# Kernel optimization log

Measured on AMD Instinct MI355X. Metric: run time of the kernel, lower is better.

The kernel has to match this reference:

```python
import jax, jax.numpy as jnp
import numpy as np


def setup_inputs() -> dict:
    key = jax.random.key(0)
    ks = jax.random.split(key, 8)
    n_videos, emb_dim = 200000, 128
    n_nodes, k_neigh = 20000, 32
    sc = 1.0 / np.sqrt(emb_dim)
    return {
        "video_embeddings": jax.random.normal(ks[0], (n_videos, emb_dim), jnp.float32),
        "video_nodes": jax.random.randint(ks[1], (n_nodes,), 0, n_videos, jnp.int64 if jax.config.jax_enable_x64 else jnp.int32),
        "neigh_idx": jax.random.randint(ks[2], (n_nodes, k_neigh), 0, n_videos, jnp.int64 if jax.config.jax_enable_x64 else jnp.int32),
        "W1": jax.random.normal(ks[3], (2 * emb_dim, emb_dim), jnp.float32) * sc,
        "b1": jnp.zeros((emb_dim,), jnp.float32),
        "W2": jax.random.normal(ks[4], (emb_dim, emb_dim), jnp.float32) * sc,
        "b2": jnp.zeros((emb_dim,), jnp.float32),
        "W3": jax.random.normal(ks[5], (emb_dim, 1), jnp.float32) * sc,
        "b3": jnp.zeros((1,), jnp.float32),
    }


def reference(video_embeddings, video_nodes, neigh_idx, W1, b1, W2, b2, W3, b3):
    # Ragged per-node loop vectorized as a padded [N, K] neighbor gather.
    neigh_emb = video_embeddings[neigh_idx]          # [N, K, D]
    node_emb = video_embeddings[video_nodes]         # [N, D]
    n, k, d = neigh_emb.shape
    # Attention MLP: cat(neigh, node_repeated) -> relu -> relu -> scalar score
    x = jnp.concatenate([neigh_emb, jnp.broadcast_to(node_emb[:, None, :], (n, k, d))], axis=-1)  # [N, K, 2D]
    h = jax.nn.relu(jnp.einsum("nke,ed->nkd", x, W1) + b1)
    h = jax.nn.relu(jnp.einsum("nke,ed->nkd", h, W2) + b2)
    scores = (jnp.einsum("nkd,do->nko", h, W3) + b3)[..., 0]  # [N, K]
    att = jax.nn.softmax(scores, axis=-1)                      # softmax over neighbors
    # Weighted aggregation: embed_matrix[i] = neigh_emb[i].T @ att[i]
    return jnp.einsum("nkd,nk->nd", neigh_emb, att)
```

## Files before the change

kernel.cpp:

```cpp
#include <hip/hip_runtime.h>
#include <hip/hip_bf16.h>

#define D  128
#define KN 32

typedef __attribute__((ext_vector_type(8))) short bf16x8;
typedef __attribute__((ext_vector_type(4))) float f32x4;

static __device__ __forceinline__ unsigned short f2bf(float f) {
    union { float f; unsigned int u; } v; v.f = f;
    unsigned int u = v.u;
    u += 0x7fff + ((u >> 16) & 1);
    return (unsigned short)(u >> 16);
}
static __device__ __forceinline__ float bf2f(unsigned short h) {
    union { float f; unsigned int u; } v; v.u = ((unsigned int)h) << 16;
    return v.f;
}

__global__ __launch_bounds__(256) void wt_kernel(
    const float* __restrict__ W1, const float* __restrict__ W2,
    unsigned short* __restrict__ W1Tt, unsigned short* __restrict__ W1Tb,
    unsigned short* __restrict__ W2T)
{
    int idx = blockIdx.x * 256 + threadIdx.x;
    if (idx < D * D) {
        int col = idx >> 7, e = idx & 127;
        W1Tt[col * D + e] = f2bf(W1[e * D + col]);
        W1Tb[col * D + e] = f2bf(W1[(D + e) * D + col]);
        W2T [col * D + e] = f2bf(W2[e * D + col]);
    }
}

__global__ __launch_bounds__(256) void p1q_kernel(
    const float* __restrict__ emb, const int* __restrict__ gidx, int M,
    const unsigned short* __restrict__ WT, const float* __restrict__ bias,
    unsigned short* __restrict__ dst)
{
    __shared__ unsigned short sA[128][136];

    const int tid  = threadIdx.x;
    const int lane = tid & 63;
    const int w    = tid >> 6;
    const int m    = lane & 15, q = lane >> 4;
    const int r0   = blockIdx.x * 128;

#pragma unroll
    for (int i = 0; i < 16; ++i) {
        int e = tid + 256 * i;
        int row = e >> 5, c4 = (e & 31) << 2;
        int r = r0 + row; if (r > M - 1) r = M - 1;
        int vr = gidx ? gidx[r] : r;
        const float4 f = *(const float4*)(emb + (long)vr * D + c4);
        ushort4 h;
        h.x = f2bf(f.x); h.y = f2bf(f.y); h.z = f2bf(f.z); h.w = f2bf(f.w);
        *(ushort4*)(&sA[row][c4]) = h;
    }
    __syncthreads();

    bf16x8 Bf[2][4];
#pragma unroll
    for (int nt = 0; nt < 2; ++nt)
#pragma unroll
        for (int kk = 0; kk < 4; ++kk)
            Bf[nt][kk] = *(const bf16x8*)(WT + (32 * w + 16 * nt + m) * D + kk * 32 + q * 8);
    float bv[2];
#pragma unroll
    for (int nt = 0; nt < 2; ++nt) bv[nt] = bias ? bias[32 * w + 16 * nt + m] : 0.f;

    f32x4 acc[8][2];
#pragma unroll
    for (int mt = 0; mt < 8; ++mt)
#pragma unroll
        for (int nt = 0; nt < 2; ++nt) acc[mt][nt] = (f32x4){0.f, 0.f, 0.f, 0.f};

#pragma unroll
    for (int kk = 0; kk < 4; ++kk) {
        bf16x8 a[8];
#pragma unroll
        for (int mt = 0; mt < 8; ++mt)
            a[mt] = *(const bf16x8*)(&sA[16 * mt + m][kk * 32 + q * 8]);
#pragma unroll
        for (int mt = 0; mt < 8; ++mt) {
            acc[mt][0] = __builtin_amdgcn_mfma_f32_16x16x32_bf16(a[mt], Bf[0][kk], acc[mt][0], 0, 0, 0);
            acc[mt][1] = __builtin_amdgcn_mfma_f32_16x16x32_bf16(a[mt], Bf[1][kk], acc[mt][1], 0, 0, 0);
        }
    }

#pragma unroll
    for (int mt = 0; mt < 8; ++mt)
#pragma unroll
        for (int nt = 0; nt < 2; ++nt) {
            int col = 32 * w + 16 * nt + m;
#pragma unroll
            for (int r = 0; r < 4; ++r) {
                int row = r0 + 16 * mt + 4 * q + r;
                if (row < M) dst[(long)row * D + col] = f2bf(acc[mt][nt][r] + bv[nt]);
            }
        }
}

__global__ __launch_bounds__(256) void agg_kernel(
    const float* __restrict__ emb,
    const int* __restrict__ nidx,
    const unsigned short* __restrict__ W2T,
    const float* __restrict__ b2, const float* __restrict__ W3,
    const float* __restrict__ b3,
    const unsigned short* __restrict__ P1, const unsigned short* __restrict__ Q,
    float* __restrict__ out, int NN)
{
    __shared__ unsigned short sX[64][136];
    __shared__ int   sIdx[64];
    __shared__ float sSp[4][64];
    __shared__ float sAtt[64];

    const int tid  = threadIdx.x;
    const int lane = tid & 63;
    const int w    = tid >> 6;
    const int m    = lane & 15, q = lane >> 4;

    bf16x8 Bf[2][4];
#pragma unroll
    for (int nt = 0; nt < 2; ++nt)
#pragma unroll
        for (int kk = 0; kk < 4; ++kk)
            Bf[nt][kk] = *(const bf16x8*)(W2T + (32 * w + 16 * nt + m) * D + kk * 32 + q * 8);
    float b2v[2], w3v[2];
#pragma unroll
    for (int nt = 0; nt < 2; ++nt) {
        int col = 32 * w + 16 * nt + m;
        b2v[nt] = b2[col];
        w3v[nt] = W3[col];
    }
    const float b3s = b3[0];

    const int pairs = (NN + 1) >> 1;
    for (int pr = blockIdx.x; pr < pairs; pr += gridDim.x) {
        const int node0 = pr * 2;

        {
            int row = tid >> 2, t4 = tid & 3;
            int nd = node0 + (row >> 5); if (nd > NN - 1) nd = NN - 1;
            int k = row & 31;
            int ni = nidx[nd * KN + k];
            if (t4 == 0) sIdx[row] = ni;
            const bf16x8* pp = (const bf16x8*)(P1 + (long)ni * D);
            const bf16x8* qq = (const bf16x8*)(Q + (long)nd * D);
#pragma unroll
            for (int j = 0; j < 4; ++j) {
                int c = t4 * 4 + j;
                bf16x8 p = pp[c], qv = qq[c], r;
#pragma unroll
                for (int h = 0; h < 8; ++h) {
                    float v = bf2f((unsigned short)p[h]) + bf2f((unsigned short)qv[h]);
                    r[h] = (short)f2bf(v > 0.f ? v : 0.f);
                }
                *(bf16x8*)(&sX[row][c * 8]) = r;
            }
        }
        __syncthreads();

        f32x4 acc[4][2];
#pragma unroll
        for (int mt = 0; mt < 4; ++mt)
#pragma unroll
            for (int nt = 0; nt < 2; ++nt) acc[mt][nt] = (f32x4){0.f, 0.f, 0.f, 0.f};

#pragma unroll
        for (int kk = 0; kk < 4; ++kk) {
            bf16x8 a[4];
#pragma unroll
            for (int mt = 0; mt < 4; ++mt)
                a[mt] = *(const bf16x8*)(&sX[16 * mt + m][kk * 32 + q * 8]);
#pragma unroll
            for (int mt = 0; mt < 4; ++mt) {
                acc[mt][0] = __builtin_amdgcn_mfma_f32_16x16x32_bf16(a[mt], Bf[0][kk], acc[mt][0], 0, 0, 0);
                acc[mt][1] = __builtin_amdgcn_mfma_f32_16x16x32_bf16(a[mt], Bf[1][kk], acc[mt][1], 0, 0, 0);
            }
        }

#pragma unroll
        for (int mt = 0; mt < 4; ++mt) {
            float p[4];
#pragma unroll
            for (int r = 0; r < 4; ++r) {
                float h0 = acc[mt][0][r] + b2v[0]; h0 = h0 > 0.f ? h0 : 0.f;
                float h1 = acc[mt][1][r] + b2v[1]; h1 = h1 > 0.f ? h1 : 0.f;
                p[r] = h0 * w3v[0] + h1 * w3v[1];
            }
#pragma unroll
            for (int off = 8; off >= 1; off >>= 1)
#pragma unroll
                for (int r = 0; r < 4; ++r) p[r] += __shfl_xor(p[r], off, 16);
            if (m == 0) {
#pragma unroll
                for (int r = 0; r < 4; ++r) sSp[w][16 * mt + 4 * q + r] = p[r];
            }
        }
        __syncthreads();

        if (tid < 64) {
            float s = sSp[0][tid] + sSp[1][tid] + sSp[2][tid] + sSp[3][tid] + b3s;
            float mx = s;
#pragma unroll
            for (int off = 16; off >= 1; off >>= 1) mx = fmaxf(mx, __shfl_xor(mx, off, 32));
            float e = __expf(s - mx);
            float sum = e;
#pragma unroll
            for (int off = 16; off >= 1; off >>= 1) sum += __shfl_xor(sum, off, 32);
            sAtt[tid] = e / sum;
        }
        __syncthreads();

        {
            int ln = tid >> 7, dcol = tid & 127;
            float a = 0.f;
#pragma unroll
            for (int k = 0; k < KN; ++k)
                a += sAtt[ln * KN + k] * emb[(long)sIdx[ln * KN + k] * D + dcol];
            int nd = node0 + ln;
            if (nd < NN) out[(long)nd * D + dcol] = a;
        }
        __syncthreads();
    }
}

__global__ __launch_bounds__(128) void naive_kernel(
    const float* __restrict__ emb, const int* __restrict__ vnodes,
    const int* __restrict__ nidx,
    const float* __restrict__ W1, const float* __restrict__ b1,
    const float* __restrict__ W2, const float* __restrict__ b2,
    const float* __restrict__ W3, const float* __restrict__ b3,
    float* __restrict__ out)
{
    __shared__ float sE[KN + 1][D];
    __shared__ float sH[KN][D];
    __shared__ float sH2[KN][D];
    __shared__ float sS[KN];
    __shared__ float sA2[KN];
    const int node = blockIdx.x, tid = threadIdx.x;

    for (int r = 0; r < KN + 1; ++r) {
        int vr = (r < KN) ? nidx[node * KN + r] : vnodes[node];
        sE[r][tid] = emb[(long)vr * D + tid];
    }
    __syncthreads();
    for (int k = 0; k < KN; ++k) {
        float s = b1[tid];
        for (int e = 0; e < D; ++e) s += sE[k][e]  * W1[e * D + tid];
        for (int e = 0; e < D; ++e) s += sE[KN][e] * W1[(D + e) * D + tid];
        sH[k][tid] = s > 0.f ? s : 0.f;
    }
    __syncthreads();
    for (int k = 0; k < KN; ++k) {
        float s = b2[tid];
        for (int e = 0; e < D; ++e) s += sH[k][e] * W2[e * D + tid];
        sH2[k][tid] = s > 0.f ? s : 0.f;
    }
    __syncthreads();
    if (tid < KN) {
        float s = b3[0];
        for (int e = 0; e < D; ++e) s += sH2[tid][e] * W3[e];
        sS[tid] = s;
    }
    __syncthreads();
    if (tid == 0) {
        float mx = sS[0];
        for (int k = 1; k < KN; ++k) mx = fmaxf(mx, sS[k]);
        float sum = 0.f;
        for (int k = 0; k < KN; ++k) { sA2[k] = __expf(sS[k] - mx); sum += sA2[k]; }
        for (int k = 0; k < KN; ++k) sA2[k] /= sum;
    }
    __syncthreads();
    float a = 0.f;
    for (int k = 0; k < KN; ++k) a += sA2[k] * sE[k][tid];
    out[(long)node * D + tid] = a;
}

extern "C" void kernel_launch(void* const* d_in, const int* in_sizes, int n_in,
                              void* d_out, int out_size, void* d_ws, size_t ws_size,
                              hipStream_t stream) {
    const float* emb    = (const float*)d_in[0];
    const int*   vnodes = (const int*)d_in[1];
    const int*   nidx   = (const int*)d_in[2];
    const float* W1     = (const float*)d_in[3];
    const float* b1     = (const float*)d_in[4];
    const float* W2     = (const float*)d_in[5];
    const float* b2     = (const float*)d_in[6];
    const float* W3     = (const float*)d_in[7];
    const float* b3     = (const float*)d_in[8];
    float* out = (float*)d_out;

    const int NV = in_sizes[0] / D;
    const int NN = in_sizes[1];

    const size_t p1_elems = (size_t)NV * D;
    const size_t q_elems  = (size_t)NN * D;
    const size_t wt_elems = (size_t)D * D;
    const size_t need = (p1_elems + q_elems + 3 * wt_elems) * sizeof(unsigned short);

    if (ws_size >= need) {
        unsigned short* P1   = (unsigned short*)d_ws;
        unsigned short* Q    = P1 + p1_elems;
        unsigned short* W1Tt = Q + q_elems;
        unsigned short* W1Tb = W1Tt + wt_elems;
        unsigned short* W2T  = W1Tb + wt_elems;
        wt_kernel<<<(D * D + 255) / 256, 256, 0, stream>>>(W1, W2, W1Tt, W1Tb, W2T);
        p1q_kernel<<<(NV + 127) / 128, 256, 0, stream>>>(emb, nullptr, NV, W1Tt, nullptr, P1);
        p1q_kernel<<<(NN + 127) / 128, 256, 0, stream>>>(emb, vnodes, NN, W1Tb, b1, Q);
        agg_kernel<<<2048, 256, 0, stream>>>(emb, nidx, W2T, b2, W3, b3, P1, Q, out, NN);
    } else {
        naive_kernel<<<NN, D, 0, stream>>>(emb, vnodes, nidx, W1, b1, W2, b2, W3, b3, out);
    }
}
```

Baseline: 325.9 us.

## Gather bf16 embedding copy in aggregation and process four nodes per block

The P1 GEMM kernel now also writes a bf16 copy of the embedding table from its shared-memory tile. The aggregation kernel gathers neighbor rows from that copy, prefetching them into registers before the MFMA stage, which halves gather bytes. The kernel now handles four nodes per block iteration with larger shared buffers and an occupancy hint. The cost is an extra 200000x128 bf16 write, more workspace, and lower-precision weighted aggregation.

```diff
diff --git a/kernel.cpp b/kernel.cpp
--- a/kernel.cpp
+++ b/kernel.cpp
@@ -35,7 +35,7 @@
 __global__ __launch_bounds__(256) void p1q_kernel(
     const float* __restrict__ emb, const int* __restrict__ gidx, int M,
     const unsigned short* __restrict__ WT, const float* __restrict__ bias,
-    unsigned short* __restrict__ dst)
+    unsigned short* __restrict__ dst, unsigned short* __restrict__ EB)
 {
     __shared__ unsigned short sA[128][136];
 
@@ -58,6 +58,16 @@
     }
     __syncthreads();
 
+    if (EB) {
+        int row = tid >> 1, half = tid & 1;
+        if (r0 + row < M) {
+#pragma unroll
+            for (int j = 0; j < 8; ++j)
+                *(bf16x8*)(EB + (long)(r0 + row) * D + half * 64 + j * 8) =
+                    *(const bf16x8*)(&sA[row][half * 64 + j * 8]);
+        }
+    }
+
     bf16x8 Bf[2][4];
 #pragma unroll
     for (int nt = 0; nt < 2; ++nt)
@@ -76,14 +86,11 @@
 
 #pragma unroll
     for (int kk = 0; kk < 4; ++kk) {
-        bf16x8 a[8];
-#pragma unroll
-        for (int mt = 0; mt < 8; ++mt)
-            a[mt] = *(const bf16x8*)(&sA[16 * mt + m][kk * 32 + q * 8]);
 #pragma unroll
         for (int mt = 0; mt < 8; ++mt) {
-            acc[mt][0] = __builtin_amdgcn_mfma_f32_16x16x32_bf16(a[mt], Bf[0][kk], acc[mt][0], 0, 0, 0);
-            acc[mt][1] = __builtin_amdgcn_mfma_f32_16x16x32_bf16(a[mt], Bf[1][kk], acc[mt][1], 0, 0, 0);
+            bf16x8 a = *(const bf16x8*)(&sA[16 * mt + m][kk * 32 + q * 8]);
+            acc[mt][0] = __builtin_amdgcn_mfma_f32_16x16x32_bf16(a, Bf[0][kk], acc[mt][0], 0, 0, 0);
+            acc[mt][1] = __builtin_amdgcn_mfma_f32_16x16x32_bf16(a, Bf[1][kk], acc[mt][1], 0, 0, 0);
         }
     }
 
@@ -100,8 +107,9 @@
         }
 }
 
-__global__ __launch_bounds__(256) void agg_kernel(
-    const float* __restrict__ emb,
+template <bool USE_EB>
+__global__ __launch_bounds__(256, 3) void agg_kernel(
+    const float* __restrict__ emb, const unsigned short* __restrict__ EB,
     const int* __restrict__ nidx,
     const unsigned short* __restrict__ W2T,
     const float* __restrict__ b2, const float* __restrict__ W3,
@@ -109,10 +117,10 @@
     const unsigned short* __restrict__ P1, const unsigned short* __restrict__ Q,
     float* __restrict__ out, int NN)
 {
-    __shared__ unsigned short sX[64][136];
-    __shared__ int   sIdx[64];
-    __shared__ float sSp[4][64];
-    __shared__ float sAtt[64];
+    __shared__ unsigned short sX[128][136];
+    __shared__ int   sIdx[128];
+    __shared__ float sSp[4][128];
+    __shared__ float sAtt[128];
 
     const int tid  = threadIdx.x;
     const int lane = tid & 63;
@@ -134,53 +142,59 @@
     }
     const float b3s = b3[0];
 
-    const int pairs = (NN + 1) >> 1;
-    for (int pr = blockIdx.x; pr < pairs; pr += gridDim.x) {
-        const int node0 = pr * 2;
+    const int groups = (NN + 3) >> 2;
+    for (int g = blockIdx.x; g < groups; g += gridDim.x) {
+        const int node0 = g * 4;
 
         {
-            int row = tid >> 2, t4 = tid & 3;
+            int row = tid >> 1, half = tid & 1;
             int nd = node0 + (row >> 5); if (nd > NN - 1) nd = NN - 1;
             int k = row & 31;
             int ni = nidx[nd * KN + k];
-            if (t4 == 0) sIdx[row] = ni;
-            const bf16x8* pp = (const bf16x8*)(P1 + (long)ni * D);
-            const bf16x8* qq = (const bf16x8*)(Q + (long)nd * D);
-#pragma unroll
-            for (int j = 0; j < 4; ++j) {
-                int c = t4 * 4 + j;
-                bf16x8 p = pp[c], qv = qq[c], r;
+            if (half == 0) sIdx[row] = ni;
+            const bf16x8* pp = (const bf16x8*)(P1 + (long)ni * D) + half * 8;
+            const bf16x8* qq = (const bf16x8*)(Q + (long)nd * D) + half * 8;
+#pragma unroll
+            for (int j = 0; j < 8; ++j) {
+                bf16x8 p = pp[j], qv = qq[j], r;
 #pragma unroll
                 for (int h = 0; h < 8; ++h) {
                     float v = bf2f((unsigned short)p[h]) + bf2f((unsigned short)qv[h]);
                     r[h] = (short)f2bf(v > 0.f ? v : 0.f);
                 }
-                *(bf16x8*)(&sX[row][c * 8]) = r;
+                *(bf16x8*)(&sX[row][half * 64 + j * 8]) = r;
             }
         }
         __syncthreads();
 
-        f32x4 acc[4][2];
-#pragma unroll
-        for (int mt = 0; mt < 4; ++mt)
+        bf16x8 gv[8];
+        if (USE_EB) {
+#pragma unroll
+            for (int j = 0; j < 8; ++j) {
+                int k = (lane >> 4) + 4 * j;
+                int ni = sIdx[w * KN + k];
+                gv[j] = *(const bf16x8*)(EB + (long)ni * D + (lane & 15) * 8);
+            }
+        }
+
+        f32x4 acc[8][2];
+#pragma unroll
+        for (int mt = 0; mt < 8; ++mt)
 #pragma unroll
             for (int nt = 0; nt < 2; ++nt) acc[mt][nt] = (f32x4){0.f, 0.f, 0.f, 0.f};
 
 #pragma unroll
         for (int kk = 0; kk < 4; ++kk) {
-            bf16x8 a[4];
-#pragma unroll
-            for (int mt = 0; mt < 4; ++mt)
-                a[mt] = *(const bf16x8*)(&sX[16 * mt + m][kk * 32 + q * 8]);
-#pragma unroll
-            for (int mt = 0; mt < 4; ++mt) {
-                acc[mt][0] = __builtin_amdgcn_mfma_f32_16x16x32_bf16(a[mt], Bf[0][kk], acc[mt][0], 0, 0, 0);
-                acc[mt][1] = __builtin_amdgcn_mfma_f32_16x16x32_bf16(a[mt], Bf[1][kk], acc[mt][1], 0, 0, 0);
-            }
-        }
-
-#pragma unroll
-        for (int mt = 0; mt < 4; ++mt) {
+#pragma unroll
+            for (int mt = 0; mt < 8; ++mt) {
+                bf16x8 a = *(const bf16x8*)(&sX[16 * mt + m][kk * 32 + q * 8]);
+                acc[mt][0] = __builtin_amdgcn_mfma_f32_16x16x32_bf16(a, Bf[0][kk], acc[mt][0], 0, 0, 0);
+                acc[mt][1] = __builtin_amdgcn_mfma_f32_16x16x32_bf16(a, Bf[1][kk], acc[mt][1], 0, 0, 0);
+            }
+        }
+
+#pragma unroll
+        for (int mt = 0; mt < 8; ++mt) {
             float p[4];
 #pragma unroll
             for (int r = 0; r < 4; ++r) {
@@ -199,7 +213,7 @@
         }
         __syncthreads();
 
-        if (tid < 64) {
+        if (tid < 128) {
             float s = sSp[0][tid] + sSp[1][tid] + sSp[2][tid] + sSp[3][tid] + b3s;
             float mx = s;
 #pragma unroll
@@ -212,14 +226,40 @@
         }
         __syncthreads();
 
-        {
-            int ln = tid >> 7, dcol = tid & 127;
-            float a = 0.f;
-#pragma unroll
-            for (int k = 0; k < KN; ++k)
-                a += sAtt[ln * KN + k] * emb[(long)sIdx[ln * KN + k] * D + dcol];
-            int nd = node0 + ln;
-            if (nd < NN) out[(long)nd * D + dcol] = a;
+        if (USE_EB) {
+            float r[8] = {0.f, 0.f, 0.f, 0.f, 0.f, 0.f, 0.f, 0.f};
+#pragma unroll
+            for (int j = 0; j < 8; ++j) {
+                float a = sAtt[w * KN + (lane >> 4) + 4 * j];
+#pragma unroll
+                for (int h = 0; h < 8; ++h)
+                    r[h] += a * bf2f((unsigned short)gv[j][h]);
+            }
+#pragma unroll
+            for (int h = 0; h < 8; ++h) {
+                r[h] += __shfl_xor(r[h], 16);
+                r[h] += __shfl_xor(r[h], 32);
+            }
+            int nd = node0 + w;
+            if (lane < 16 && nd < NN) {
+                float4 o0 = {r[0], r[1], r[2], r[3]};
+                float4 o1 = {r[4], r[5], r[6], r[7]};
+                *(float4*)(out + (long)nd * D + lane * 8)     = o0;
+                *(float4*)(out + (long)nd * D + lane * 8 + 4) = o1;
+            }
+        } else {
+            float a0 = 0.f, a1 = 0.f;
+            for (int k = 0; k < KN; ++k) {
+                float att = sAtt[w * KN + k];
+                const float* er = emb + (long)sIdx[w * KN + k] * D;
+                a0 += att * er[lane];
+                a1 += att * er[lane + 64];
+            }
+            int nd = node0 + w;
+            if (nd < NN) {
+                out[(long)nd * D + lane]      = a0;
+                out[(long)nd * D + lane + 64] = a1;
+            }
         }
         __syncthreads();
     }
@@ -297,18 +337,25 @@
     const size_t p1_elems = (size_t)NV * D;
     const size_t q_elems  = (size_t)NN * D;
     const size_t wt_elems = (size_t)D * D;
-    const size_t need = (p1_elems + q_elems + 3 * wt_elems) * sizeof(unsigned short);
-
-    if (ws_size >= need) {
+    const size_t base_elems = p1_elems + q_elems + 3 * wt_elems;
+    const size_t need_base = base_elems * sizeof(unsigned short);
+    const size_t need_eb   = (base_elems + p1_elems) * sizeof(unsigned short);
+
+    if (ws_size >= need_base) {
         unsigned short* P1   = (unsigned short*)d_ws;
         unsigned short* Q    = P1 + p1_elems;
         unsigned short* W1Tt = Q + q_elems;
         unsigned short* W1Tb = W1Tt + wt_elems;
         unsigned short* W2T  = W1Tb + wt_elems;
+        unsigned short* EB   = (ws_size >= need_eb) ? (W2T + wt_elems) : nullptr;
+
         wt_kernel<<<(D * D + 255) / 256, 256, 0, stream>>>(W1, W2, W1Tt, W1Tb, W2T);
-        p1q_kernel<<<(NV + 127) / 128, 256, 0, stream>>>(emb, nullptr, NV, W1Tt, nullptr, P1);
-        p1q_kernel<<<(NN + 127) / 128, 256, 0, stream>>>(emb, vnodes, NN, W1Tb, b1, Q);
-        agg_kernel<<<2048, 256, 0, stream>>>(emb, nidx, W2T, b2, W3, b3, P1, Q, out, NN);
+        p1q_kernel<<<(NV + 127) / 128, 256, 0, stream>>>(emb, nullptr, NV, W1Tt, nullptr, P1, EB);
+        p1q_kernel<<<(NN + 127) / 128, 256, 0, stream>>>(emb, vnodes, NN, W1Tb, b1, Q, nullptr);
+        if (EB)
+            agg_kernel<true><<<2048, 256, 0, stream>>>(emb, EB, nidx, W2T, b2, W3, b3, P1, Q, out, NN);
+        else
+            agg_kernel<false><<<2048, 256, 0, stream>>>(emb, nullptr, nidx, W2T, b2, W3, b3, P1, Q, out, NN);
     } else {
         naive_kernel<<<NN, D, 0, stream>>>(emb, vnodes, nidx, W1, b1, W2, b2, W3, b3, out);
     }
```

New measurement: 315.4 us. -3.2%, faster.

## Merge projection launches, emit bf16 embeddings, and process one node per wave

Applied to the files above, without the earlier changes.

The two projection launches are merged into a single grid. The NV branch also writes a bf16 copy of the embedding table, and the A tiles are loaded straight from global memory instead of going through shared memory. The aggregation kernel now gives each wave its own node, so it needs no shared memory or block barriers. The softmax and weighted sum run entirely in registers with shuffles, and the weighted sum reads the half-size bf16 embeddings. This cuts fp32 gather traffic and synchronisation, at the cost of an extra bf16 table write, bf16 precision in the aggregation, and dropping b3 (harmless, since softmax is shift-invariant).

```diff
diff --git a/kernel.cpp b/kernel.cpp
--- a/kernel.cpp
+++ b/kernel.cpp
@@ -16,6 +16,12 @@
 static __device__ __forceinline__ float bf2f(unsigned short h) {
     union { float f; unsigned int u; } v; v.u = ((unsigned int)h) << 16;
     return v.f;
+}
+static __device__ __forceinline__ float bflo(unsigned int u) {
+    union { float f; unsigned int u; } v; v.u = u << 16; return v.f;
+}
+static __device__ __forceinline__ float bfhi(unsigned int u) {
+    union { float f; unsigned int u; } v; v.u = u & 0xffff0000u; return v.f;
 }
 
 __global__ __launch_bounds__(256) void wt_kernel(
@@ -33,196 +39,189 @@
 }
 
 __global__ __launch_bounds__(256) void p1q_kernel(
-    const float* __restrict__ emb, const int* __restrict__ gidx, int M,
-    const unsigned short* __restrict__ WT, const float* __restrict__ bias,
-    unsigned short* __restrict__ dst)
+    const float* __restrict__ emb, const int* __restrict__ vnodes,
+    int NV, int NN, int nvBlocks,
+    const unsigned short* __restrict__ W1Tt, const unsigned short* __restrict__ W1Tb,
+    const float* __restrict__ b1,
+    unsigned short* __restrict__ P1, unsigned short* __restrict__ Q,
+    unsigned short* __restrict__ EB)
 {
-    __shared__ unsigned short sA[128][136];
-
     const int tid  = threadIdx.x;
     const int lane = tid & 63;
     const int w    = tid >> 6;
     const int m    = lane & 15, q = lane >> 4;
-    const int r0   = blockIdx.x * 128;
-
-#pragma unroll
-    for (int i = 0; i < 16; ++i) {
-        int e = tid + 256 * i;
-        int row = e >> 5, c4 = (e & 31) << 2;
-        int r = r0 + row; if (r > M - 1) r = M - 1;
-        int vr = gidx ? gidx[r] : r;
-        const float4 f = *(const float4*)(emb + (long)vr * D + c4);
-        ushort4 h;
-        h.x = f2bf(f.x); h.y = f2bf(f.y); h.z = f2bf(f.z); h.w = f2bf(f.w);
-        *(ushort4*)(&sA[row][c4]) = h;
-    }
-    __syncthreads();
-
-    bf16x8 Bf[2][4];
-#pragma unroll
-    for (int nt = 0; nt < 2; ++nt)
-#pragma unroll
-        for (int kk = 0; kk < 4; ++kk)
-            Bf[nt][kk] = *(const bf16x8*)(WT + (32 * w + 16 * nt + m) * D + kk * 32 + q * 8);
-    float bv[2];
-#pragma unroll
-    for (int nt = 0; nt < 2; ++nt) bv[nt] = bias ? bias[32 * w + 16 * nt + m] : 0.f;
-
-    f32x4 acc[8][2];
-#pragma unroll
-    for (int mt = 0; mt < 8; ++mt)
-#pragma unroll
-        for (int nt = 0; nt < 2; ++nt) acc[mt][nt] = (f32x4){0.f, 0.f, 0.f, 0.f};
+
+    const bool nv = (int)blockIdx.x < nvBlocks;
+    const int  bi = nv ? blockIdx.x : blockIdx.x - nvBlocks;
+    const int  M  = nv ? NV : NN;
+    const unsigned short* WT = nv ? W1Tt : W1Tb;
+    unsigned short* dst = nv ? P1 : Q;
+    const int r0w = bi * 128 + w * 32;
+
+    int row[2], vr[2];
+#pragma unroll
+    for (int mt = 0; mt < 2; ++mt) {
+        int r = r0w + 16 * mt + m;
+        row[mt] = r < M ? r : M - 1;
+        vr[mt]  = nv ? row[mt] : vnodes[row[mt]];
+    }
+
+    f32x4 acc[2][8];
+#pragma unroll
+    for (int mt = 0; mt < 2; ++mt)
+#pragma unroll
+        for (int nt = 0; nt < 8; ++nt) acc[mt][nt] = (f32x4){0.f, 0.f, 0.f, 0.f};
 
 #pragma unroll
     for (int kk = 0; kk < 4; ++kk) {
-        bf16x8 a[8];
-#pragma unroll
-        for (int mt = 0; mt < 8; ++mt)
-            a[mt] = *(const bf16x8*)(&sA[16 * mt + m][kk * 32 + q * 8]);
-#pragma unroll
-        for (int mt = 0; mt < 8; ++mt) {
-            acc[mt][0] = __builtin_amdgcn_mfma_f32_16x16x32_bf16(a[mt], Bf[0][kk], acc[mt][0], 0, 0, 0);
-            acc[mt][1] = __builtin_amdgcn_mfma_f32_16x16x32_bf16(a[mt], Bf[1][kk], acc[mt][1], 0, 0, 0);
-        }
-    }
-
-#pragma unroll
-    for (int mt = 0; mt < 8; ++mt)
-#pragma unroll
-        for (int nt = 0; nt < 2; ++nt) {
-            int col = 32 * w + 16 * nt + m;
+        bf16x8 a[2];
+#pragma unroll
+        for (int mt = 0; mt < 2; ++mt) {
+            const float* src = emb + (long)vr[mt] * D + kk * 32 + q * 8;
+            float4 f0 = *(const float4*)src;
+            float4 f1 = *(const float4*)(src + 4);
+            a[mt][0] = (short)f2bf(f0.x); a[mt][1] = (short)f2bf(f0.y);
+            a[mt][2] = (short)f2bf(f0.z); a[mt][3] = (short)f2bf(f0.w);
+            a[mt][4] = (short)f2bf(f1.x); a[mt][5] = (short)f2bf(f1.y);
+            a[mt][6] = (short)f2bf(f1.z); a[mt][7] = (short)f2bf(f1.w);
+            if (nv && EB)
+                *(bf16x8*)(EB + (long)row[mt] * D + kk * 32 + q * 8) = a[mt];
+        }
+#pragma unroll
+        for (int nt = 0; nt < 8; ++nt) {
+            bf16x8 b = *(const bf16x8*)(WT + (16 * nt + m) * D + kk * 32 + q * 8);
+            acc[0][nt] = __builtin_amdgcn_mfma_f32_16x16x32_bf16(a[0], b, acc[0][nt], 0, 0, 0);
+            acc[1][nt] = __builtin_amdgcn_mfma_f32_16x16x32_bf16(a[1], b, acc[1][nt], 0, 0, 0);
+        }
+    }
+
+    float bv[8];
+#pragma unroll
+    for (int nt = 0; nt < 8; ++nt) bv[nt] = nv ? 0.f : b1[16 * nt + m];
+
+#pragma unroll
+    for (int mt = 0; mt < 2; ++mt)
+#pragma unroll
+        for (int nt = 0; nt < 8; ++nt)
 #pragma unroll
             for (int r = 0; r < 4; ++r) {
-                int row = r0 + 16 * mt + 4 * q + r;
-                if (row < M) dst[(long)row * D + col] = f2bf(acc[mt][nt][r] + bv[nt]);
+                int orow = r0w + 16 * mt + 4 * q + r;
+                if (orow < M)
+                    dst[(long)orow * D + 16 * nt + m] = f2bf(acc[mt][nt][r] + bv[nt]);
             }
-        }
 }
 
 __global__ __launch_bounds__(256) void agg_kernel(
-    const float* __restrict__ emb,
-    const int* __restrict__ nidx,
-    const unsigned short* __restrict__ W2T,
-    const float* __restrict__ b2, const float* __restrict__ W3,
-    const float* __restrict__ b3,
+    const unsigned short* __restrict__ EB, const int* __restrict__ nidx,
+    const unsigned short* __restrict__ W2T, const float* __restrict__ b2,
+    const float* __restrict__ W3,
     const unsigned short* __restrict__ P1, const unsigned short* __restrict__ Q,
     float* __restrict__ out, int NN)
 {
-    __shared__ unsigned short sX[64][136];
-    __shared__ int   sIdx[64];
-    __shared__ float sSp[4][64];
-    __shared__ float sAtt[64];
-
-    const int tid  = threadIdx.x;
-    const int lane = tid & 63;
-    const int w    = tid >> 6;
+    const int lane = threadIdx.x & 63;
+    const int w    = threadIdx.x >> 6;
     const int m    = lane & 15, q = lane >> 4;
-
-    bf16x8 Bf[2][4];
-#pragma unroll
-    for (int nt = 0; nt < 2; ++nt)
-#pragma unroll
-        for (int kk = 0; kk < 4; ++kk)
-            Bf[nt][kk] = *(const bf16x8*)(W2T + (32 * w + 16 * nt + m) * D + kk * 32 + q * 8);
-    float b2v[2], w3v[2];
-#pragma unroll
-    for (int nt = 0; nt < 2; ++nt) {
-        int col = 32 * w + 16 * nt + m;
-        b2v[nt] = b2[col];
-        w3v[nt] = W3[col];
-    }
-    const float b3s = b3[0];
-
-    const int pairs = (NN + 1) >> 1;
-    for (int pr = blockIdx.x; pr < pairs; pr += gridDim.x) {
-        const int node0 = pr * 2;
-
-        {
-            int row = tid >> 2, t4 = tid & 3;
-            int nd = node0 + (row >> 5); if (nd > NN - 1) nd = NN - 1;
-            int k = row & 31;
-            int ni = nidx[nd * KN + k];
-            if (t4 == 0) sIdx[row] = ni;
-            const bf16x8* pp = (const bf16x8*)(P1 + (long)ni * D);
-            const bf16x8* qq = (const bf16x8*)(Q + (long)nd * D);
-#pragma unroll
-            for (int j = 0; j < 4; ++j) {
-                int c = t4 * 4 + j;
-                bf16x8 p = pp[c], qv = qq[c], r;
-#pragma unroll
-                for (int h = 0; h < 8; ++h) {
-                    float v = bf2f((unsigned short)p[h]) + bf2f((unsigned short)qv[h]);
-                    r[h] = (short)f2bf(v > 0.f ? v : 0.f);
-                }
-                *(bf16x8*)(&sX[row][c * 8]) = r;
+    const int nd   = blockIdx.x * 4 + w;
+    if (nd >= NN) return;
+
+    const int idxv = nidx[nd * KN + (lane & 31)];
+    const int r0 = __shfl(idxv, m);
+    const int r1 = __shfl(idxv, 16 + m);
+
+    unsigned int ek[KN];
+#pragma unroll
+    for (int k = 0; k < KN; ++k) {
+        int ik = __shfl(idxv, k);
+        ek[k] = *(const unsigned int*)(EB + (long)ik * D + lane * 2);
+    }
+
+    float b2v[8], w3v[8];
+#pragma unroll
+    for (int nt = 0; nt < 8; ++nt) {
+        b2v[nt] = b2[16 * nt + m];
+        w3v[nt] = W3[16 * nt + m];
+    }
+
+    f32x4 acc[2][8];
+#pragma unroll
+    for (int mt = 0; mt < 2; ++mt)
+#pragma unroll
+        for (int nt = 0; nt < 8; ++nt) acc[mt][nt] = (f32x4){0.f, 0.f, 0.f, 0.f};
+
+#pragma unroll
+    for (int kk = 0; kk < 4; ++kk) {
+        bf16x8 qv = *(const bf16x8*)(Q  + (long)nd * D + kk * 32 + q * 8);
+        bf16x8 p0 = *(const bf16x8*)(P1 + (long)r0 * D + kk * 32 + q * 8);
+        bf16x8 p1 = *(const bf16x8*)(P1 + (long)r1 * D + kk * 32 + q * 8);
+        bf16x8 a0, a1;
+#pragma unroll
+        for (int h = 0; h < 8; ++h) {
+            float v0 = bf2f((unsigned short)p0[h]) + bf2f((unsigned short)qv[h]);
+            float v1 = bf2f((unsigned short)p1[h]) + bf2f((unsigned short)qv[h]);
+            a0[h] = (short)f2bf(v0 > 0.f ? v0 : 0.f);
+            a1[h] = (short)f2bf(v1 > 0.f ? v1 : 0.f);
+        }
+#pragma unroll
+        for (int nt = 0; nt < 8; ++nt) {
+            bf16x8 b = *(const bf16x8*)(W2T + (16 * nt + m) * D + kk * 32 + q * 8);
+            acc[0][nt] = __builtin_amdgcn_mfma_f32_16x16x32_bf16(a0, b, acc[0][nt], 0, 0, 0);
+            acc[1][nt] = __builtin_amdgcn_mfma_f32_16x16x32_bf16(a1, b, acc[1][nt], 0, 0, 0);
+        }
+    }
+
+    float att[2][4];
+#pragma unroll
+    for (int mt = 0; mt < 2; ++mt)
+#pragma unroll
+        for (int r = 0; r < 4; ++r) {
+            float p = 0.f;
+#pragma unroll
+            for (int nt = 0; nt < 8; ++nt) {
+                float h = acc[mt][nt][r] + b2v[nt];
+                p += (h > 0.f ? h : 0.f) * w3v[nt];
             }
-        }
-        __syncthreads();
-
-        f32x4 acc[4][2];
-#pragma unroll
-        for (int mt = 0; mt < 4; ++mt)
-#pragma unroll
-            for (int nt = 0; nt < 2; ++nt) acc[mt][nt] = (f32x4){0.f, 0.f, 0.f, 0.f};
-
-#pragma unroll
-        for (int kk = 0; kk < 4; ++kk) {
-            bf16x8 a[4];
-#pragma unroll
-            for (int mt = 0; mt < 4; ++mt)
-                a[mt] = *(const bf16x8*)(&sX[16 * mt + m][kk * 32 + q * 8]);
-#pragma unroll
-            for (int mt = 0; mt < 4; ++mt) {
-                acc[mt][0] = __builtin_amdgcn_mfma_f32_16x16x32_bf16(a[mt], Bf[0][kk], acc[mt][0], 0, 0, 0);
-                acc[mt][1] = __builtin_amdgcn_mfma_f32_16x16x32_bf16(a[mt], Bf[1][kk], acc[mt][1], 0, 0, 0);
-            }
-        }
-
-#pragma unroll
-        for (int mt = 0; mt < 4; ++mt) {
-            float p[4];
-#pragma unroll
-            for (int r = 0; r < 4; ++r) {
-                float h0 = acc[mt][0][r] + b2v[0]; h0 = h0 > 0.f ? h0 : 0.f;
-                float h1 = acc[mt][1][r] + b2v[1]; h1 = h1 > 0.f ? h1 : 0.f;
-                p[r] = h0 * w3v[0] + h1 * w3v[1];
-            }
-#pragma unroll
-            for (int off = 8; off >= 1; off >>= 1)
-#pragma unroll
-                for (int r = 0; r < 4; ++r) p[r] += __shfl_xor(p[r], off, 16);
-            if (m == 0) {
-#pragma unroll
-                for (int r = 0; r < 4; ++r) sSp[w][16 * mt + 4 * q + r] = p[r];
-            }
-        }
-        __syncthreads();
-
-        if (tid < 64) {
-            float s = sSp[0][tid] + sSp[1][tid] + sSp[2][tid] + sSp[3][tid] + b3s;
-            float mx = s;
-#pragma unroll
-            for (int off = 16; off >= 1; off >>= 1) mx = fmaxf(mx, __shfl_xor(mx, off, 32));
-            float e = __expf(s - mx);
-            float sum = e;
-#pragma unroll
-            for (int off = 16; off >= 1; off >>= 1) sum += __shfl_xor(sum, off, 32);
-            sAtt[tid] = e / sum;
-        }
-        __syncthreads();
-
-        {
-            int ln = tid >> 7, dcol = tid & 127;
-            float a = 0.f;
-#pragma unroll
-            for (int k = 0; k < KN; ++k)
-                a += sAtt[ln * KN + k] * emb[(long)sIdx[ln * KN + k] * D + dcol];
-            int nd = node0 + ln;
-            if (nd < NN) out[(long)nd * D + dcol] = a;
-        }
-        __syncthreads();
-    }
+            att[mt][r] = p;
+        }
+#pragma unroll
+    for (int off = 1; off <= 8; off <<= 1)
+#pragma unroll
+        for (int mt = 0; mt < 2; ++mt)
+#pragma unroll
+            for (int r = 0; r < 4; ++r)
+                att[mt][r] += __shfl_xor(att[mt][r], off);
+
+    float mx = att[0][0];
+#pragma unroll
+    for (int mt = 0; mt < 2; ++mt)
+#pragma unroll
+        for (int r = 0; r < 4; ++r) mx = fmaxf(mx, att[mt][r]);
+    mx = fmaxf(mx, __shfl_xor(mx, 16));
+    mx = fmaxf(mx, __shfl_xor(mx, 32));
+    float sum = 0.f;
+#pragma unroll
+    for (int mt = 0; mt < 2; ++mt)
+#pragma unroll
+        for (int r = 0; r < 4; ++r) {
+            att[mt][r] = __expf(att[mt][r] - mx);
+            sum += att[mt][r];
+        }
+    sum += __shfl_xor(sum, 16);
+    sum += __shfl_xor(sum, 32);
+    const float inv = 1.f / sum;
+#pragma unroll
+    for (int mt = 0; mt < 2; ++mt)
+#pragma unroll
+        for (int r = 0; r < 4; ++r) att[mt][r] *= inv;
+
+    float ox = 0.f, oy = 0.f;
+#pragma unroll
+    for (int k = 0; k < KN; ++k) {
+        float a = __shfl(att[k >> 4][k & 3], ((k >> 2) & 3) << 4);
+        ox += a * bflo(ek[k]);
+        oy += a * bfhi(ek[k]);
+    }
+    float2 o = {ox, oy};
+    *(float2*)(out + (long)nd * D + lane * 2) = o;
 }
 
 __global__ __launch_bounds__(128) void naive_kernel(
@@ -297,7 +296,7 @@
     const size_t p1_elems = (size_t)NV * D;
     const size_t q_elems  = (size_t)NN * D;
     const size_t wt_elems = (size_t)D * D;
-    const size_t need = (p1_elems + q_elems + 3 * wt_elems) * sizeof(unsigned short);
+    const size_t need = (2 * p1_elems + q_elems + 3 * wt_elems) * sizeof(unsigned short);
 
     if (ws_size >= need) {
         unsigned short* P1   = (unsigned short*)d_ws;
@@ -305,10 +304,16 @@
         unsigned short* W1Tt = Q + q_elems;
         unsigned short* W1Tb = W1Tt + wt_elems;
         unsigned short* W2T  = W1Tb + wt_elems;
+        unsigned short* EB   = W2T + wt_elems;
+
+        const int nvBlocks = (NV + 127) / 128;
+        const int qBlocks  = (NN + 127) / 128;
+
         wt_kernel<<<(D * D + 255) / 256, 256, 0, stream>>>(W1, W2, W1Tt, W1Tb, W2T);
-        p1q_kernel<<<(NV + 127) / 128, 256, 0, stream>>>(emb, nullptr, NV, W1Tt, nullptr, P1);
-        p1q_kernel<<<(NN + 127) / 128, 256, 0, stream>>>(emb, vnodes, NN, W1Tb, b1, Q);
-        agg_kernel<<<2048, 256, 0, stream>>>(emb, nidx, W2T, b2, W3, b3, P1, Q, out, NN);
+        p1q_kernel<<<nvBlocks + qBlocks, 256, 0, stream>>>(
+            emb, vnodes, NV, NN, nvBlocks, W1Tt, W1Tb, b1, P1, Q, EB);
+        agg_kernel<<<(NN + 3) / 4, 256, 0, stream>>>(
+            EB, nidx, W2T, b2, W3, P1, Q, out, NN);
     } else {
         naive_kernel<<<NN, D, 0, stream>>>(emb, vnodes, nidx, W1, b1, W2, b2, W3, b3, out);
     }
```

Result: slower. 349.3 us (+7.2%).
